# Kernel tuning notes

Hardware: AMD Instinct MI355X
Metric: run time of the kernel (lower is better)

## Reference

```python
import jax, jax.numpy as jnp
import numpy as np

B, C, N, K = 4, 256, 8192, 16
H, S = 8, 2            # num_heads, num_scale
HC = C // H            # head_channels = 32
CS = C // S            # per-scale channels = 128
HS = H // S            # heads per scale = 4
KV_CH = (64, 128)
EPS = 1e-5
SCALE = HC ** -0.5


def setup_inputs() -> dict:
    key = jax.random.key(0)
    ks = jax.random.split(key, 20)
    d = {}
    d["x"] = jax.random.normal(ks[0], (B, C, N), jnp.float32)
    d["y0"] = jax.random.normal(ks[1], (B, KV_CH[0], N, K), jnp.float32)
    d["y1"] = jax.random.normal(ks[2], (B, KV_CH[1], N, K), jnp.float32)
    d["q_w"] = jax.random.normal(ks[3], (C, C), jnp.float32) * 0.02
    for i, c in enumerate(KV_CH):
        kk = jax.random.split(ks[4 + i], 4)
        d[f"conv{i}_w"] = jax.random.normal(kk[0], (CS, c), jnp.float32) * 0.05  # 1x1 conv
        d[f"bn{i}_g"] = jnp.ones((CS,), jnp.float32)
        d[f"bn{i}_b"] = jnp.zeros((CS,), jnp.float32)
        d[f"bn{i}_m"] = jax.random.normal(kk[1], (CS,), jnp.float32) * 0.1
        d[f"bn{i}_v"] = jax.random.uniform(kk[2], (CS,), jnp.float32) + 0.5
        d[f"kv{i}_w"] = jax.random.normal(kk[3], (2 * CS, CS), jnp.float32) * 0.02
    d["proj_w"] = jax.random.normal(ks[8], (C, C), jnp.float32) * 0.02
    d["proj_b"] = jnp.zeros((C,), jnp.float32)
    return d


def _scale_branch(q_i, y, conv_w, g, b, m, v, kv_w):
    # q_i: [B, HS, N, HC];  y: [B, c, N, K]
    z = jnp.einsum('bcnk,oc->bonk', y, conv_w)                 # 1x1 conv -> [B, CS, N, K]
    inv = (g / jnp.sqrt(v + EPS))[None, :, None, None]
    z = jax.nn.relu((z - m[None, :, None, None]) * inv + b[None, :, None, None])
    kv = jnp.transpose(z, (0, 2, 3, 1)) @ kv_w.T               # [B, N, K, 2*CS]
    kv = kv.reshape(B, N, K, HS, HC, 2)
    k = jnp.transpose(kv[..., 0], (0, 3, 1, 2, 4))             # [B, HS, N, K, HC]
    vv = jnp.transpose(kv[..., 1], (0, 3, 1, 2, 4))            # [B, HS, N, K, HC]
    attn = jax.nn.softmax(jnp.einsum('bhnd,bhnkd->bhnk', q_i, k) * SCALE, axis=-1)
    out = jnp.einsum('bhnk,bhnkd->bhnd', attn, vv)             # [B, HS, N, HC]
    return jnp.transpose(out, (0, 2, 1, 3)).reshape(B, N, HS * HC)


def reference(x, y0, y1, q_w,
              conv0_w, bn0_g, bn0_b, bn0_m, bn0_v, kv0_w,
              conv1_w, bn1_g, bn1_b, bn1_m, bn1_v, kv1_w,
              proj_w, proj_b):
    xt = jnp.swapaxes(x, 1, 2)                                 # [B, N, C]
    q = (xt @ q_w.T).reshape(B, N, H, HC).transpose(0, 2, 1, 3)  # [B, H, N, HC]
    o0 = _scale_branch(q[:, :HS], y0, conv0_w, bn0_g, bn0_b, bn0_m, bn0_v, kv0_w)
    o1 = _scale_branch(q[:, HS:], y1, conv1_w, bn1_g, bn1_b, bn1_m, bn1_v, kv1_w)
    outs = jnp.concatenate([o0, o1], axis=-1)                  # [B, N, C]
    outs = outs @ proj_w.T + proj_b
    return jnp.swapaxes(outs, 1, 2)                            # [B, C, N]
```

## Files before the change

kernel.cpp:

```cpp
#include <hip/hip_runtime.h>
#include <hip/hip_bf16.h>

typedef __attribute__((ext_vector_type(8))) short bf16x8;
typedef __attribute__((ext_vector_type(4))) short bf16x4;
typedef __attribute__((ext_vector_type(4))) float f32x4;
typedef unsigned short ushort_t;
typedef unsigned int uint_t;

__device__ __forceinline__ f32x4 mfma32(bf16x8 a, bf16x8 b, f32x4 c) {
    return __builtin_amdgcn_mfma_f32_16x16x32_bf16(a, b, c, 0, 0, 0);
}
#if __has_builtin(__builtin_amdgcn_mfma_f32_16x16x16bf16_1k)
#define HAVE_MFMA16 1
__device__ __forceinline__ f32x4 mfma16(bf16x4 a, bf16x4 b, f32x4 c) {
    return __builtin_amdgcn_mfma_f32_16x16x16bf16_1k(a, b, c, 0, 0, 0);
}
#else
#define HAVE_MFMA16 0
#endif

__device__ __forceinline__ void softbar() {
    asm volatile("s_waitcnt lgkmcnt(0)" ::: "memory");
    __builtin_amdgcn_s_barrier();
}

namespace {
constexpr int Bn = 4;
constexpr int Nn = 8192;
constexpr float SCALEf = 0.17677669529663687f;
constexpr float EPSf = 1e-5f;

constexpr size_t WS_QW  = 0;
constexpr size_t WS_PW  = 131072;
constexpr size_t WS_KW0 = 262144;
constexpr size_t WS_KW1 = 327680;
constexpr size_t WS_CW0 = 393216;
constexpr size_t WS_CW1 = 409600;
constexpr size_t WS_CB0 = 442368;
constexpr size_t WS_CB1 = 442880;
constexpr size_t WS_AO  = 458752;
}

__device__ __forceinline__ uint_t f2b(float f) {
    union { float f; uint_t u; } v; v.f = f;
    return (v.u + 0x7fffu + ((v.u >> 16) & 1u)) >> 16;
}
__device__ __forceinline__ float b2f(ushort_t u) {
    union { uint_t u; float f; } v; v.u = ((uint_t)u) << 16;
    return v.f;
}
__device__ __forceinline__ uint_t pk2(float lo, float hi) {
    __hip_bfloat162 h = __float22bfloat162_rn(float2{lo, hi});
    union { __hip_bfloat162 h; uint_t u; } v; v.h = h;
    return v.u;
}

template<int KC>
__device__ __forceinline__ int swz(int r, int c) {
    constexpr int SW = (KC / 8 < 16 ? KC / 8 : 16);
    return r * KC + ((((c >> 3) ^ (r & (SW - 1))) << 3) | (c & 7));
}

__global__ void plsa_prep(const float* __restrict__ qw,
                          const float* __restrict__ c0w, const float* __restrict__ g0,
                          const float* __restrict__ b0,  const float* __restrict__ m0,
                          const float* __restrict__ v0,  const float* __restrict__ k0w,
                          const float* __restrict__ c1w, const float* __restrict__ g1,
                          const float* __restrict__ b1,  const float* __restrict__ m1,
                          const float* __restrict__ v1,  const float* __restrict__ k1w,
                          const float* __restrict__ pw,  char* ws) {
    const int i = blockIdx.x * 256 + threadIdx.x;
    ((ushort_t*)(ws + WS_QW))[i] = (ushort_t)f2b(qw[i]);
    ((ushort_t*)(ws + WS_PW))[i] = (ushort_t)f2b(pw[i]);
    if (i < 32768) {
        ((ushort_t*)(ws + WS_KW0))[i] = (ushort_t)f2b(k0w[i]);
        ((ushort_t*)(ws + WS_KW1))[i] = (ushort_t)f2b(k1w[i]);
    }
    if (i < 8192)  { int o = i >> 6;  float inv = g0[o] * rsqrtf(v0[o] + EPSf);
                     ((ushort_t*)(ws + WS_CW0))[i] = (ushort_t)f2b(c0w[i] * inv); }
    if (i < 16384) { int o = i >> 7;  float inv = g1[o] * rsqrtf(v1[o] + EPSf);
                     ((ushort_t*)(ws + WS_CW1))[i] = (ushort_t)f2b(c1w[i] * inv); }
    if (i < 128) {
        float i0 = g0[i] * rsqrtf(v0[i] + EPSf);
        float i1 = g1[i] * rsqrtf(v1[i] + EPSf);
        ((float*)(ws + WS_CB0))[i] = b0[i] - m0[i] * i0;
        ((float*)(ws + WS_CB1))[i] = b1[i] - m1[i] * i1;
    }
}

template<int CIN>
__device__ __forceinline__ void issue_y2(const float* __restrict__ yb, int b, int n0c,
                                         float* yreg, int tid) {
    constexpr int ITER = CIN / 16;
    #pragma unroll
    for (int it = 0; it < ITER; ++it) {
        const int idx = tid + it * 256;
        const int pk = idx & 31, c0 = (idx >> 5) * 2;
        const float* ysrc = yb + ((size_t)(b * CIN + c0)) * (Nn * 16)
                               + (size_t)(n0c + (pk >> 4)) * 16 + (pk & 15);
        yreg[it * 2]     = ysrc[0];
        yreg[it * 2 + 1] = ysrc[(size_t)Nn * 16];
    }
}
template<int CIN>
__device__ __forceinline__ void write_y2(ushort_t* Ys, const float* yreg, int tid) {
    constexpr int ITER = CIN / 16;
    #pragma unroll
    for (int it = 0; it < ITER; ++it) {
        const int idx = tid + it * 256;
        const int pk = idx & 31, c0 = (idx >> 5) * 2;
        *(uint_t*)(Ys + swz<CIN>(pk, c0)) = pk2(yreg[it * 2], yreg[it * 2 + 1]);
    }
}

template<int CIN, int NCIN>
__device__ __forceinline__ void branch_run(
    int tid, int b, int n0,
    const float* __restrict__ yb, const float* __restrict__ ynext,
    const char* __restrict__ ws,
    ushort_t* Ys, ushort_t* Zs, ushort_t* Ks, ushort_t* Vs,
    const ushort_t* qs, ushort_t* aobuf, float* yreg)
{
    constexpr size_t wcw = (CIN == 64) ? WS_CW0 : WS_CW1;
    constexpr size_t wcb = (CIN == 64) ? WS_CB0 : WS_CB1;
    constexpr size_t wkw = (CIN == 64) ? WS_KW0 : WS_KW1;
    constexpr int qb = (CIN == 64) ? 0 : 128;
    constexpr int KT = CIN / 32;

    const ushort_t* cwb = (const ushort_t*)(ws + wcw);
    const float*    cbb = (const float*)(ws + wcb);
    const ushort_t* kwb = (const ushort_t*)(ws + wkw);
    const int w = tid >> 6, lane = tid & 63, l15 = lane & 15, lk = lane >> 4;

    bf16x8 cwf[2 * KT]; float4 cbv[2];
    #pragma unroll
    for (int mi = 0; mi < 2; ++mi) {
        #pragma unroll
        for (int k = 0; k < KT; ++k)
            cwf[mi * KT + k] = *(const bf16x8*)(cwb + ((w * 2 + mi) * 16 + l15) * CIN + k * 32 + lk * 8);
        cbv[mi] = *(const float4*)(cbb + (w * 2 + mi) * 16 + lk * 4);
    }
    bf16x8 kwf[16];
    #pragma unroll
    for (int mi = 0; mi < 4; ++mi)
        #pragma unroll
        for (int k = 0; k < 4; ++k)
            kwf[mi * 4 + k] = *(const bf16x8*)(kwb + ((w * 4 + mi) * 16 + l15) * 128 + k * 32 + lk * 8);

    #pragma unroll 1
    for (int cc = 0; cc < 8; ++cc) {
        #pragma unroll
        for (int ct = 0; ct < 2; ++ct) {
            bf16x8 bfr[KT];
            #pragma unroll
            for (int k = 0; k < KT; ++k)
                bfr[k] = *(const bf16x8*)(Ys + swz<CIN>(ct * 16 + l15, k * 32 + lk * 8));
            #pragma unroll
            for (int mi = 0; mi < 2; ++mi) {
                f32x4 a = f32x4{0.f, 0.f, 0.f, 0.f};
                #pragma unroll
                for (int k = 0; k < KT; ++k)
                    a = mfma32(cwf[mi * KT + k], bfr[k], a);
                const int col = ct * 16 + l15, o0 = (w * 2 + mi) * 16 + lk * 4;
                const float z0 = fmaxf(a.x + cbv[mi].x, 0.f);
                const float z1 = fmaxf(a.y + cbv[mi].y, 0.f);
                const float z2 = fmaxf(a.z + cbv[mi].z, 0.f);
                const float z3 = fmaxf(a.w + cbv[mi].w, 0.f);
                const int off = swz<128>(col, o0);
                *(uint_t*)(Zs + off)     = pk2(z0, z1);
                *(uint_t*)(Zs + off + 2) = pk2(z2, z3);
            }
        }
        softbar();

        #pragma unroll
        for (int ct = 0; ct < 2; ++ct) {
            bf16x8 bfr[4];
            #pragma unroll
            for (int k = 0; k < 4; ++k)
                bfr[k] = *(const bf16x8*)(Zs + swz<128>(ct * 16 + l15, k * 32 + lk * 8));
            const int col = ct * 16 + l15;
            #pragma unroll
            for (int mi = 0; mi < 4; ++mi) {
                f32x4 a = f32x4{0.f, 0.f, 0.f, 0.f};
                #pragma unroll
                for (int k = 0; k < 4; ++k)
                    a = mfma32(kwf[mi * 4 + k], bfr[k], a);
                const int j0 = (w * 4 + mi) * 16 + lk * 4;
                const int h = j0 >> 6;
                const int d0 = (j0 & 63) >> 1;
                *(uint_t*)(Ks + swz<128>(col, h * 32 + d0)) = pk2(a.x, a.z);
                const uint_t vv = pk2(a.y, a.w);
                Vs[swz<32>(h * 32 + d0,     col)] = (ushort_t)vv;
                Vs[swz<32>(h * 32 + d0 + 1, col)] = (ushort_t)(vv >> 16);
            }
        }
        if (cc < 7) write_y2<CIN>(Ys, yreg, tid);
        else if constexpr (NCIN != 0) write_y2<NCIN>(Ys, yreg, tid);
        if (cc < 6) issue_y2<CIN>(yb, b, n0 + (cc + 2) * 2, yreg, tid);
        else if (cc == 6) { if constexpr (NCIN != 0) issue_y2<NCIN>(ynext, b, n0, yreg, tid); }
        else              { if constexpr (NCIN != 0) issue_y2<NCIN>(ynext, b, n0 + 2, yreg, tid); }
        softbar();

#if HAVE_MFMA16
        {
            const int pt = w >> 1, pr = w & 1;
            #pragma unroll
            for (int hh = 0; hh < 2; ++hh) {
                const int h = pr * 2 + hh;
                bf16x8 ka  = *(const bf16x8*)(Ks + swz<128>(pt * 16 + l15, h * 32 + lk * 8));
                bf16x8 qf  = *(const bf16x8*)(qs + swz<256>(cc * 2 + pt, qb + h * 32 + lk * 8));
                f32x4 zero = f32x4{0.f, 0.f, 0.f, 0.f};
                f32x4 sc = mfma32(ka, qf, zero);
                float s0 = sc.x * SCALEf, s1 = sc.y * SCALEf;
                float s2 = sc.z * SCALEf, s3 = sc.w * SCALEf;
                float mx = fmaxf(fmaxf(s0, s1), fmaxf(s2, s3));
                mx = fmaxf(mx, __shfl_xor(mx, 16));
                mx = fmaxf(mx, __shfl_xor(mx, 32));
                float e0 = __expf(s0 - mx), e1 = __expf(s1 - mx);
                float e2 = __expf(s2 - mx), e3 = __expf(s3 - mx);
                float t = e0 + e1 + e2 + e3;
                t += __shfl_xor(t, 16);
                t += __shfl_xor(t, 32);
                const float r = 1.f / t;
                union { uint_t u[2]; bf16x4 v; } pf;
                pf.u[0] = pk2(e0 * r, e1 * r);
                pf.u[1] = pk2(e2 * r, e3 * r);
                #pragma unroll
                for (int dblk = 0; dblk < 2; ++dblk) {
                    bf16x4 va = *(const bf16x4*)(Vs + swz<32>(h * 32 + dblk * 16 + l15, pt * 16 + lk * 4));
                    f32x4 o = mfma16(va, pf.v, zero);
                    if (l15 == 0) {
                        uint2 ou;
                        ou.x = pk2(o.x, o.y);
                        ou.y = pk2(o.z, o.w);
                        *(uint2*)(aobuf + ((size_t)(b * Nn + n0 + cc * 2 + pt)) * 256
                                  + qb + h * 32 + dblk * 16 + lk * 4) = ou;
                    }
                }
            }
        }
#else
        {
            const int pt = w >> 1, pr = w & 1;
            float p = 0.f;
            if (lane < 32) {
                const int kk = lane & 15;
                const int h = pr * 2 + (lane >> 4);
                float s = 0.f;
                #pragma unroll
                for (int dc = 0; dc < 4; ++dc) {
                    bf16x8 q8 = *(const bf16x8*)(qs + swz<256>(cc * 2 + pt, qb + h * 32 + dc * 8));
                    bf16x8 k8 = *(const bf16x8*)(Ks + swz<128>(pt * 16 + kk, h * 32 + dc * 8));
                    #pragma unroll
                    for (int j = 0; j < 8; ++j)
                        s += b2f((ushort_t)q8[j]) * b2f((ushort_t)k8[j]);
                }
                s *= SCALEf;
                float mx = s;
                #pragma unroll
                for (int m = 1; m < 16; m <<= 1) mx = fmaxf(mx, __shfl_xor(mx, m));
                const float e = __expf(s - mx);
                float sum = e;
                #pragma unroll
                for (int m = 1; m < 16; m <<= 1) sum += __shfl_xor(sum, m);
                p = e / sum;
            }
            const int d = lane & 31, hh2 = lane >> 5;
            const int h2 = pr * 2 + hh2;
            const int row = h2 * 32 + d;
            bf16x8 va = *(const bf16x8*)(Vs + swz<32>(row, pt * 16));
            bf16x8 vb = *(const bf16x8*)(Vs + swz<32>(row, pt * 16 + 8));
            float o = 0.f;
            #pragma unroll
            for (int j = 0; j < 8; ++j) {
                o += __shfl(p, hh2 * 16 + j)     * b2f((ushort_t)va[j]);
                o += __shfl(p, hh2 * 16 + 8 + j) * b2f((ushort_t)vb[j]);
            }
            aobuf[((size_t)(b * Nn + n0 + cc * 2 + pt)) * 256 + qb + h2 * 32 + d] = (ushort_t)f2b(o);
        }
#endif
    }
}

__global__ __launch_bounds__(256, 2) void k_attn(
    const float* __restrict__ x, const float* __restrict__ y0, const float* __restrict__ y1,
    const char* __restrict__ ws, ushort_t* __restrict__ aobuf) {

    __shared__ __align__(16) ushort_t qs[4096];
    __shared__ __align__(16) ushort_t Ys[4096];
    __shared__ __align__(16) ushort_t Zs[4096];
    __shared__ __align__(16) ushort_t Ks[4096];
    __shared__ __align__(16) ushort_t Vs[4096];

    const int tid = threadIdx.x;
    const int b = blockIdx.x >> 9, n0 = (blockIdx.x & 511) << 4;
    const int w = tid >> 6, lane = tid & 63, l15 = lane & 15, lk = lane >> 4;
    float yreg[16];

    const int xn = tid & 15, cg = tid >> 4;
    #pragma unroll
    for (int hseg = 0; hseg < 2; ++hseg) {
        float xreg[8];
        #pragma unroll
        for (int i = 0; i < 8; ++i)
            xreg[i] = x[((size_t)(b * 256 + cg * 16 + hseg * 8 + i)) * Nn + n0 + xn];
        #pragma unroll
        for (int j = 0; j < 4; ++j)
            *(uint_t*)(Ys + swz<256>(xn, cg * 16 + hseg * 8 + 2 * j)) =
                pk2(xreg[2 * j], xreg[2 * j + 1]);
    }
    issue_y2<64>(y0, b, n0, yreg, tid);
    __syncthreads();

    {
        const ushort_t* qwb = (const ushort_t*)(ws + WS_QW);
        #pragma unroll
        for (int mi = 0; mi < 4; ++mi) {
            f32x4 acc = f32x4{0.f, 0.f, 0.f, 0.f};
            #pragma unroll
            for (int k = 0; k < 8; ++k) {
                bf16x8 af = *(const bf16x8*)(qwb + ((w * 4 + mi) * 16 + l15) * 256 + k * 32 + lk * 8);
                bf16x8 bf = *(const bf16x8*)(Ys + swz<256>(l15, k * 32 + lk * 8));
                acc = mfma32(af, bf, acc);
            }
            const int ch0 = (w * 4 + mi) * 16 + lk * 4;
            uint2 u;
            u.x = pk2(acc.x, acc.y);
            u.y = pk2(acc.z, acc.w);
            *(uint2*)(qs + swz<256>(l15, ch0)) = u;
        }
    }
    __syncthreads();

    write_y2<64>(Ys, yreg, tid);
    issue_y2<64>(y0, b, n0 + 2, yreg, tid);
    __syncthreads();

    branch_run<64, 128>(tid, b, n0, y0, y1, ws, Ys, Zs, Ks, Vs, qs, aobuf, yreg);
    branch_run<128, 0> (tid, b, n0, y1, nullptr, ws, Ys, Zs, Ks, Vs, qs, aobuf, yreg);
}

__global__ __launch_bounds__(256, 2) void k_proj(const char* __restrict__ ws,
                                                 const float* __restrict__ proj_b,
                                                 float* __restrict__ out) {
    __shared__ __align__(16) ushort_t At[64 * 256];
    const ushort_t* pwb = (const ushort_t*)(ws + WS_PW);
    const ushort_t* aobuf = (const ushort_t*)(ws + WS_AO);
    const int tid = threadIdx.x;
    const int b = blockIdx.x >> 7, n0 = (blockIdx.x & 127) * 64;

    {
        const int cp = tid & 127, ng = tid >> 7;
        #pragma unroll
        for (int i = 0; i < 32; ++i) {
            const int n = ng + i * 2;
            const uint_t u = *(const uint_t*)(aobuf + ((size_t)(b * Nn + n0 + n)) * 256 + cp * 2);
            *(uint_t*)(At + swz<256>(n, cp * 2)) = u;
        }
    }
    __syncthreads();

    const int w = tid >> 6, lane = tid & 63, l15 = lane & 15, lk = lane >> 4;
    #pragma unroll
    for (int mi = 0; mi < 4; ++mi) {
        bf16x8 af[8];
        #pragma unroll
        for (int k = 0; k < 8; ++k)
            af[k] = *(const bf16x8*)(pwb + (w * 64 + mi * 16 + l15) * 256 + k * 32 + lk * 8);
        const int ch0 = w * 64 + mi * 16 + lk * 4;
        const float4 pbv = *(const float4*)(proj_b + ch0);
        #pragma unroll
        for (int ct = 0; ct < 4; ++ct) {
            f32x4 acc = f32x4{0.f, 0.f, 0.f, 0.f};
            #pragma unroll
            for (int k = 0; k < 8; ++k) {
                bf16x8 bf = *(const bf16x8*)(At + swz<256>(ct * 16 + l15, k * 32 + lk * 8));
                acc = mfma32(af[k], bf, acc);
            }
            const int nn = n0 + ct * 16 + l15;
            out[((size_t)(b * 256 + ch0 + 0)) * Nn + nn] = acc.x + pbv.x;
            out[((size_t)(b * 256 + ch0 + 1)) * Nn + nn] = acc.y + pbv.y;
            out[((size_t)(b * 256 + ch0 + 2)) * Nn + nn] = acc.z + pbv.z;
            out[((size_t)(b * 256 + ch0 + 3)) * Nn + nn] = acc.w + pbv.w;
        }
    }
}

extern "C" void kernel_launch(void* const* d_in, const int* in_sizes, int n_in,
                              void* d_out, int out_size, void* d_ws, size_t ws_size,
                              hipStream_t stream) {
    const float* x       = (const float*)d_in[0];
    const float* y0      = (const float*)d_in[1];
    const float* y1      = (const float*)d_in[2];
    const float* q_w     = (const float*)d_in[3];
    const float* conv0_w = (const float*)d_in[4];
    const float* bn0_g   = (const float*)d_in[5];
    const float* bn0_b   = (const float*)d_in[6];
    const float* bn0_m   = (const float*)d_in[7];
    const float* bn0_v   = (const float*)d_in[8];
    const float* kv0_w   = (const float*)d_in[9];
    const float* conv1_w = (const float*)d_in[10];
    const float* bn1_g   = (const float*)d_in[11];
    const float* bn1_b   = (const float*)d_in[12];
    const float* bn1_m   = (const float*)d_in[13];
    const float* bn1_v   = (const float*)d_in[14];
    const float* kv1_w   = (const float*)d_in[15];
    const float* proj_w  = (const float*)d_in[16];
    const float* proj_b  = (const float*)d_in[17];
    char* ws = (char*)d_ws;

    plsa_prep<<<256, 256, 0, stream>>>(q_w, conv0_w, bn0_g, bn0_b, bn0_m, bn0_v, kv0_w,
                                       conv1_w, bn1_g, bn1_b, bn1_m, bn1_v, kv1_w,
                                       proj_w, ws);
    k_attn<<<Bn * (Nn / 16), 256, 0, stream>>>(x, y0, y1, ws,
                                               (ushort_t*)(ws + WS_AO));
    k_proj<<<Bn * (Nn / 64), 256, 0, stream>>>(ws, proj_b, (float*)d_out);
}
```

Baseline: 295.0 us.

## Double-buffer LDS stages and skew conv/kv/attention phases across iterations

Result: faster. 276.8 us (-6.2%).

```diff
diff --git a/kernel.cpp b/kernel.cpp
--- a/kernel.cpp
+++ b/kernel.cpp
@@ -29,6 +29,7 @@
 constexpr int Nn = 8192;
 constexpr float SCALEf = 0.17677669529663687f;
 constexpr float EPSf = 1e-5f;
+constexpr int BUF = 4096;
 
 constexpr size_t WS_QW  = 0;
 constexpr size_t WS_PW  = 131072;
@@ -103,14 +104,149 @@
     }
 }
 template<int CIN>
-__device__ __forceinline__ void write_y2(ushort_t* Ys, const float* yreg, int tid) {
+__device__ __forceinline__ void write_y2(ushort_t* Ysb, const float* yreg, int tid) {
     constexpr int ITER = CIN / 16;
     #pragma unroll
     for (int it = 0; it < ITER; ++it) {
         const int idx = tid + it * 256;
         const int pk = idx & 31, c0 = (idx >> 5) * 2;
-        *(uint_t*)(Ys + swz<CIN>(pk, c0)) = pk2(yreg[it * 2], yreg[it * 2 + 1]);
-    }
+        *(uint_t*)(Ysb + swz<CIN>(pk, c0)) = pk2(yreg[it * 2], yreg[it * 2 + 1]);
+    }
+}
+
+template<int CIN>
+__device__ __forceinline__ void phaseA(int l15, int lk, int w,
+    const ushort_t* Ysb, ushort_t* Zsb, const bf16x8* cwf, const float4* cbv) {
+    constexpr int KT = CIN / 32;
+    #pragma unroll
+    for (int ct = 0; ct < 2; ++ct) {
+        bf16x8 bfr[KT];
+        #pragma unroll
+        for (int k = 0; k < KT; ++k)
+            bfr[k] = *(const bf16x8*)(Ysb + swz<CIN>(ct * 16 + l15, k * 32 + lk * 8));
+        #pragma unroll
+        for (int mi = 0; mi < 2; ++mi) {
+            f32x4 a = f32x4{0.f, 0.f, 0.f, 0.f};
+            #pragma unroll
+            for (int k = 0; k < KT; ++k)
+                a = mfma32(cwf[mi * KT + k], bfr[k], a);
+            const int col = ct * 16 + l15, o0 = (w * 2 + mi) * 16 + lk * 4;
+            const float z0 = fmaxf(a.x + cbv[mi].x, 0.f);
+            const float z1 = fmaxf(a.y + cbv[mi].y, 0.f);
+            const float z2 = fmaxf(a.z + cbv[mi].z, 0.f);
+            const float z3 = fmaxf(a.w + cbv[mi].w, 0.f);
+            const int off = swz<128>(col, o0);
+            *(uint_t*)(Zsb + off)     = pk2(z0, z1);
+            *(uint_t*)(Zsb + off + 2) = pk2(z2, z3);
+        }
+    }
+}
+
+__device__ __forceinline__ void phaseB(int l15, int lk, int w,
+    const ushort_t* Zsb, ushort_t* Ksb, ushort_t* Vsb, const bf16x8* kwf) {
+    #pragma unroll
+    for (int ct = 0; ct < 2; ++ct) {
+        bf16x8 bfr[4];
+        #pragma unroll
+        for (int k = 0; k < 4; ++k)
+            bfr[k] = *(const bf16x8*)(Zsb + swz<128>(ct * 16 + l15, k * 32 + lk * 8));
+        const int col = ct * 16 + l15;
+        #pragma unroll
+        for (int mi = 0; mi < 4; ++mi) {
+            f32x4 a = f32x4{0.f, 0.f, 0.f, 0.f};
+            #pragma unroll
+            for (int k = 0; k < 4; ++k)
+                a = mfma32(kwf[mi * 4 + k], bfr[k], a);
+            const int j0 = (w * 4 + mi) * 16 + lk * 4;
+            const int h = j0 >> 6;
+            const int d0 = (j0 & 63) >> 1;
+            *(uint_t*)(Ksb + swz<128>(col, h * 32 + d0)) = pk2(a.x, a.z);
+            const uint_t vv = pk2(a.y, a.w);
+            Vsb[swz<32>(h * 32 + d0,     col)] = (ushort_t)vv;
+            Vsb[swz<32>(h * 32 + d0 + 1, col)] = (ushort_t)(vv >> 16);
+        }
+    }
+}
+
+template<int QB>
+__device__ __forceinline__ void phaseC(int j, int tid, int b, int n0,
+    const ushort_t* Ksb, const ushort_t* Vsb, const ushort_t* qs,
+    ushort_t* __restrict__ aobuf) {
+    const int w = tid >> 6, lane = tid & 63, l15 = lane & 15, lk = lane >> 4;
+#if HAVE_MFMA16
+    const int pt = w >> 1, pr = w & 1;
+    #pragma unroll
+    for (int hh = 0; hh < 2; ++hh) {
+        const int h = pr * 2 + hh;
+        bf16x8 ka  = *(const bf16x8*)(Ksb + swz<128>(pt * 16 + l15, h * 32 + lk * 8));
+        bf16x8 qf  = *(const bf16x8*)(qs + swz<256>(j * 2 + pt, QB + h * 32 + lk * 8));
+        f32x4 zero = f32x4{0.f, 0.f, 0.f, 0.f};
+        f32x4 sc = mfma32(ka, qf, zero);
+        float s0 = sc.x * SCALEf, s1 = sc.y * SCALEf;
+        float s2 = sc.z * SCALEf, s3 = sc.w * SCALEf;
+        float mx = fmaxf(fmaxf(s0, s1), fmaxf(s2, s3));
+        mx = fmaxf(mx, __shfl_xor(mx, 16));
+        mx = fmaxf(mx, __shfl_xor(mx, 32));
+        float e0 = __expf(s0 - mx), e1 = __expf(s1 - mx);
+        float e2 = __expf(s2 - mx), e3 = __expf(s3 - mx);
+        float t = e0 + e1 + e2 + e3;
+        t += __shfl_xor(t, 16);
+        t += __shfl_xor(t, 32);
+        const float r = 1.f / t;
+        union { uint_t u[2]; bf16x4 v; } pf;
+        pf.u[0] = pk2(e0 * r, e1 * r);
+        pf.u[1] = pk2(e2 * r, e3 * r);
+        #pragma unroll
+        for (int dblk = 0; dblk < 2; ++dblk) {
+            bf16x4 va = *(const bf16x4*)(Vsb + swz<32>(h * 32 + dblk * 16 + l15, pt * 16 + lk * 4));
+            f32x4 o = mfma16(va, pf.v, zero);
+            if (l15 == 0) {
+                uint2 ou;
+                ou.x = pk2(o.x, o.y);
+                ou.y = pk2(o.z, o.w);
+                *(uint2*)(aobuf + ((size_t)(b * Nn + n0 + j * 2 + pt)) * 256
+                          + QB + h * 32 + dblk * 16 + lk * 4) = ou;
+            }
+        }
+    }
+#else
+    const int pt = w >> 1, pr = w & 1;
+    float p = 0.f;
+    if (lane < 32) {
+        const int kk = lane & 15;
+        const int h = pr * 2 + (lane >> 4);
+        float s = 0.f;
+        #pragma unroll
+        for (int dc = 0; dc < 4; ++dc) {
+            bf16x8 q8 = *(const bf16x8*)(qs + swz<256>(j * 2 + pt, QB + h * 32 + dc * 8));
+            bf16x8 k8 = *(const bf16x8*)(Ksb + swz<128>(pt * 16 + kk, h * 32 + dc * 8));
+            #pragma unroll
+            for (int jj = 0; jj < 8; ++jj)
+                s += b2f((ushort_t)q8[jj]) * b2f((ushort_t)k8[jj]);
+        }
+        s *= SCALEf;
+        float mx = s;
+        #pragma unroll
+        for (int m = 1; m < 16; m <<= 1) mx = fmaxf(mx, __shfl_xor(mx, m));
+        const float e = __expf(s - mx);
+        float sum = e;
+        #pragma unroll
+        for (int m = 1; m < 16; m <<= 1) sum += __shfl_xor(sum, m);
+        p = e / sum;
+    }
+    const int d = lane & 31, hh2 = lane >> 5;
+    const int h2 = pr * 2 + hh2;
+    const int row = h2 * 32 + d;
+    bf16x8 va = *(const bf16x8*)(Vsb + swz<32>(row, pt * 16));
+    bf16x8 vb = *(const bf16x8*)(Vsb + swz<32>(row, pt * 16 + 8));
+    float o = 0.f;
+    #pragma unroll
+    for (int jj = 0; jj < 8; ++jj) {
+        o += __shfl(p, hh2 * 16 + jj)     * b2f((ushort_t)va[jj]);
+        o += __shfl(p, hh2 * 16 + 8 + jj) * b2f((ushort_t)vb[jj]);
+    }
+    aobuf[((size_t)(b * Nn + n0 + j * 2 + pt)) * 256 + QB + h2 * 32 + d] = (ushort_t)f2b(o);
+#endif
 }
 
 template<int CIN, int NCIN>
@@ -124,7 +260,7 @@
     constexpr size_t wcw = (CIN == 64) ? WS_CW0 : WS_CW1;
     constexpr size_t wcb = (CIN == 64) ? WS_CB0 : WS_CB1;
     constexpr size_t wkw = (CIN == 64) ? WS_KW0 : WS_KW1;
-    constexpr int qb = (CIN == 64) ? 0 : 128;
+    constexpr int QB = (CIN == 64) ? 0 : 128;
     constexpr int KT = CIN / 32;
 
     const ushort_t* cwb = (const ushort_t*)(ws + wcw);
@@ -147,140 +283,23 @@
         for (int k = 0; k < 4; ++k)
             kwf[mi * 4 + k] = *(const bf16x8*)(kwb + ((w * 4 + mi) * 16 + l15) * 128 + k * 32 + lk * 8);
 
+    phaseA<CIN>(l15, lk, w, Ys, Zs, cwf, cbv);
+    softbar();
+
     #pragma unroll 1
     for (int cc = 0; cc < 8; ++cc) {
-        #pragma unroll
-        for (int ct = 0; ct < 2; ++ct) {
-            bf16x8 bfr[KT];
-            #pragma unroll
-            for (int k = 0; k < KT; ++k)
-                bfr[k] = *(const bf16x8*)(Ys + swz<CIN>(ct * 16 + l15, k * 32 + lk * 8));
-            #pragma unroll
-            for (int mi = 0; mi < 2; ++mi) {
-                f32x4 a = f32x4{0.f, 0.f, 0.f, 0.f};
-                #pragma unroll
-                for (int k = 0; k < KT; ++k)
-                    a = mfma32(cwf[mi * KT + k], bfr[k], a);
-                const int col = ct * 16 + l15, o0 = (w * 2 + mi) * 16 + lk * 4;
-                const float z0 = fmaxf(a.x + cbv[mi].x, 0.f);
-                const float z1 = fmaxf(a.y + cbv[mi].y, 0.f);
-                const float z2 = fmaxf(a.z + cbv[mi].z, 0.f);
-                const float z3 = fmaxf(a.w + cbv[mi].w, 0.f);
-                const int off = swz<128>(col, o0);
-                *(uint_t*)(Zs + off)     = pk2(z0, z1);
-                *(uint_t*)(Zs + off + 2) = pk2(z2, z3);
-            }
-        }
+        const int p  = cc & 1;
+        const int pn = p ^ 1;
+        phaseB(l15, lk, w, Zs + p * BUF, Ks + p * BUF, Vs + p * BUF, kwf);
+        if (cc >= 1) phaseC<QB>(cc - 1, tid, b, n0, Ks + pn * BUF, Vs + pn * BUF, qs, aobuf);
+        if (cc <= 6) phaseA<CIN>(l15, lk, w, Ys + pn * BUF, Zs + pn * BUF, cwf, cbv);
+        if (cc <= 5) write_y2<CIN>(Ys + p * BUF, yreg, tid);
+        else if constexpr (NCIN != 0) { write_y2<NCIN>(Ys + p * BUF, yreg, tid); }
+        if (cc <= 4) issue_y2<CIN>(yb, b, n0 + (cc + 3) * 2, yreg, tid);
+        else if constexpr (NCIN != 0) { issue_y2<NCIN>(ynext, b, n0 + (cc - 5) * 2, yreg, tid); }
         softbar();
-
-        #pragma unroll
-        for (int ct = 0; ct < 2; ++ct) {
-            bf16x8 bfr[4];
-            #pragma unroll
-            for (int k = 0; k < 4; ++k)
-                bfr[k] = *(const bf16x8*)(Zs + swz<128>(ct * 16 + l15, k * 32 + lk * 8));
-            const int col = ct * 16 + l15;
-            #pragma unroll
-            for (int mi = 0; mi < 4; ++mi) {
-                f32x4 a = f32x4{0.f, 0.f, 0.f, 0.f};
-                #pragma unroll
-                for (int k = 0; k < 4; ++k)
-                    a = mfma32(kwf[mi * 4 + k], bfr[k], a);
-                const int j0 = (w * 4 + mi) * 16 + lk * 4;
-                const int h = j0 >> 6;
-                const int d0 = (j0 & 63) >> 1;
-                *(uint_t*)(Ks + swz<128>(col, h * 32 + d0)) = pk2(a.x, a.z);
-                const uint_t vv = pk2(a.y, a.w);
-                Vs[swz<32>(h * 32 + d0,     col)] = (ushort_t)vv;
-                Vs[swz<32>(h * 32 + d0 + 1, col)] = (ushort_t)(vv >> 16);
-            }
-        }
-        if (cc < 7) write_y2<CIN>(Ys, yreg, tid);
-        else if constexpr (NCIN != 0) write_y2<NCIN>(Ys, yreg, tid);
-        if (cc < 6) issue_y2<CIN>(yb, b, n0 + (cc + 2) * 2, yreg, tid);
-        else if (cc == 6) { if constexpr (NCIN != 0) issue_y2<NCIN>(ynext, b, n0, yreg, tid); }
-        else              { if constexpr (NCIN != 0) issue_y2<NCIN>(ynext, b, n0 + 2, yreg, tid); }
-        softbar();
-
-#if HAVE_MFMA16
-        {
-            const int pt = w >> 1, pr = w & 1;
-            #pragma unroll
-            for (int hh = 0; hh < 2; ++hh) {
-                const int h = pr * 2 + hh;
-                bf16x8 ka  = *(const bf16x8*)(Ks + swz<128>(pt * 16 + l15, h * 32 + lk * 8));
-                bf16x8 qf  = *(const bf16x8*)(qs + swz<256>(cc * 2 + pt, qb + h * 32 + lk * 8));
-                f32x4 zero = f32x4{0.f, 0.f, 0.f, 0.f};
-                f32x4 sc = mfma32(ka, qf, zero);
-                float s0 = sc.x * SCALEf, s1 = sc.y * SCALEf;
-                float s2 = sc.z * SCALEf, s3 = sc.w * SCALEf;
-                float mx = fmaxf(fmaxf(s0, s1), fmaxf(s2, s3));
-                mx = fmaxf(mx, __shfl_xor(mx, 16));
-                mx = fmaxf(mx, __shfl_xor(mx, 32));
-                float e0 = __expf(s0 - mx), e1 = __expf(s1 - mx);
-                float e2 = __expf(s2 - mx), e3 = __expf(s3 - mx);
-                float t = e0 + e1 + e2 + e3;
-                t += __shfl_xor(t, 16);
-                t += __shfl_xor(t, 32);
-                const float r = 1.f / t;
-                union { uint_t u[2]; bf16x4 v; } pf;
-                pf.u[0] = pk2(e0 * r, e1 * r);
-                pf.u[1] = pk2(e2 * r, e3 * r);
-                #pragma unroll
-                for (int dblk = 0; dblk < 2; ++dblk) {
-                    bf16x4 va = *(const bf16x4*)(Vs + swz<32>(h * 32 + dblk * 16 + l15, pt * 16 + lk * 4));
-                    f32x4 o = mfma16(va, pf.v, zero);
-                    if (l15 == 0) {
-                        uint2 ou;
-                        ou.x = pk2(o.x, o.y);
-                        ou.y = pk2(o.z, o.w);
-                        *(uint2*)(aobuf + ((size_t)(b * Nn + n0 + cc * 2 + pt)) * 256
-                                  + qb + h * 32 + dblk * 16 + lk * 4) = ou;
-                    }
-                }
-            }
-        }
-#else
-        {
-            const int pt = w >> 1, pr = w & 1;
-            float p = 0.f;
-            if (lane < 32) {
-                const int kk = lane & 15;
-                const int h = pr * 2 + (lane >> 4);
-                float s = 0.f;
-                #pragma unroll
-                for (int dc = 0; dc < 4; ++dc) {
-                    bf16x8 q8 = *(const bf16x8*)(qs + swz<256>(cc * 2 + pt, qb + h * 32 + dc * 8));
-                    bf16x8 k8 = *(const bf16x8*)(Ks + swz<128>(pt * 16 + kk, h * 32 + dc * 8));
-                    #pragma unroll
-                    for (int j = 0; j < 8; ++j)
-                        s += b2f((ushort_t)q8[j]) * b2f((ushort_t)k8[j]);
-                }
-                s *= SCALEf;
-                float mx = s;
-                #pragma unroll
-                for (int m = 1; m < 16; m <<= 1) mx = fmaxf(mx, __shfl_xor(mx, m));
-                const float e = __expf(s - mx);
-                float sum = e;
-                #pragma unroll
-                for (int m = 1; m < 16; m <<= 1) sum += __shfl_xor(sum, m);
-                p = e / sum;
-            }
-            const int d = lane & 31, hh2 = lane >> 5;
-            const int h2 = pr * 2 + hh2;
-            const int row = h2 * 32 + d;
-            bf16x8 va = *(const bf16x8*)(Vs + swz<32>(row, pt * 16));
-            bf16x8 vb = *(const bf16x8*)(Vs + swz<32>(row, pt * 16 + 8));
-            float o = 0.f;
-            #pragma unroll
-            for (int j = 0; j < 8; ++j) {
-                o += __shfl(p, hh2 * 16 + j)     * b2f((ushort_t)va[j]);
-                o += __shfl(p, hh2 * 16 + 8 + j) * b2f((ushort_t)vb[j]);
-            }
-            aobuf[((size_t)(b * Nn + n0 + cc * 2 + pt)) * 256 + qb + h2 * 32 + d] = (ushort_t)f2b(o);
-        }
-#endif
-    }
+    }
+    phaseC<QB>(7, tid, b, n0, Ks + BUF, Vs + BUF, qs, aobuf);
 }
 
 __global__ __launch_bounds__(256, 2) void k_attn(
@@ -288,10 +307,10 @@
     const char* __restrict__ ws, ushort_t* __restrict__ aobuf) {
 
     __shared__ __align__(16) ushort_t qs[4096];
-    __shared__ __align__(16) ushort_t Ys[4096];
-    __shared__ __align__(16) ushort_t Zs[4096];
-    __shared__ __align__(16) ushort_t Ks[4096];
-    __shared__ __align__(16) ushort_t Vs[4096];
+    __shared__ __align__(16) ushort_t Ys[2 * BUF];
+    __shared__ __align__(16) ushort_t Zs[2 * BUF];
+    __shared__ __align__(16) ushort_t Ks[2 * BUF];
+    __shared__ __align__(16) ushort_t Vs[2 * BUF];
 
     const int tid = threadIdx.x;
     const int b = blockIdx.x >> 9, n0 = (blockIdx.x & 511) << 4;
@@ -335,7 +354,10 @@
 
     write_y2<64>(Ys, yreg, tid);
     issue_y2<64>(y0, b, n0 + 2, yreg, tid);
-    __syncthreads();
+    softbar();
+    write_y2<64>(Ys + BUF, yreg, tid);
+    issue_y2<64>(y0, b, n0 + 4, yreg, tid);
+    softbar();
 
     branch_run<64, 128>(tid, b, n0, y0, y1, ws, Ys, Zs, Ks, Vs, qs, aobuf, yreg);
     branch_run<128, 0> (tid, b, n0, y1, nullptr, ws, Ys, Zs, Ks, Vs, qs, aobuf, yreg);
```
